# Kernel optimization log

Measured on AMD Instinct MI355X. Metric: run time of the kernel, lower is better.

The kernel has to match this reference:

```python
import jax, jax.numpy as jnp
import numpy as np

N_NODES = 100000
K_NBRS = 16
N_EDGES = N_NODES * K_NBRS


def setup_inputs() -> dict:
    key = jax.random.key(0)
    ks = jax.random.split(key, 20)
    x = jax.random.normal(ks[0], (N_NODES, 3), dtype=jnp.float32)
    # knn-like edge list: every node is the target of exactly K_NBRS edges
    dst = jnp.repeat(jnp.arange(N_NODES, dtype=jnp.int64), K_NBRS)
    src = jax.random.randint(ks[1], (N_EDGES,), 0, N_NODES, dtype=jnp.int64)
    edge_index = jnp.stack([src, dst], axis=0)  # [2, E], row0=source(j), row1=target(i)

    def lin_init(k, fan_in, fan_out):
        s = 1.0 / np.sqrt(fan_in)
        return jax.random.uniform(k, (fan_in, fan_out), jnp.float32, -s, s)

    inp = {"x": x, "edge_index": edge_index}
    inp["W1"], inp["b1"] = lin_init(ks[2], 6, 64), jnp.zeros((64,), jnp.float32)
    for i, kk in zip(range(2, 6), ks[3:7]):
        inp[f"W{i}"] = lin_init(kk, 128, 64)
        inp[f"b{i}"] = jnp.zeros((64,), jnp.float32)
    inp["Wa"], inp["ba"] = lin_init(ks[8], 128, 128), jnp.zeros((128,), jnp.float32)
    inp["Wb"], inp["bb"] = lin_init(ks[9], 128, 3), jnp.zeros((3,), jnp.float32)
    return inp


def edge_conv(x, src, dst, W, b):
    # PyG EdgeConv: message = nn(cat([x_i, x_j - x_i])), max-aggregate at target i
    xi = x[dst]                      # [E, C] center (target) features
    xj = x[src]                      # [E, C] neighbor (source) features
    msg = jnp.concatenate([xi, xj - xi], axis=-1)  # [E, 2C]
    msg = jax.nn.relu(msg @ W + b)                 # [E, 64] per-edge MLP
    return jax.ops.segment_max(msg, dst, num_segments=N_NODES)  # [N, 64]


def reference(x, edge_index, W1, b1, W2, b2, W3, b3, W4, b4, W5, b5, Wa, ba, Wb, bb):
    src, dst = edge_index[0], edge_index[1]
    h = edge_conv(x, src, dst, W1, b1)
    h = edge_conv(h, src, dst, W2, b2)
    h = edge_conv(h, src, dst, W3, b3)
    h = edge_conv(h, src, dst, W4, b4)
    h = edge_conv(h, src, dst, W5, b5)           # [N, 64]
    g = jnp.max(h, axis=0, keepdims=True)        # [1, 64] global max
    feat = jnp.concatenate([h, jnp.broadcast_to(g, h.shape)], axis=1)  # [N, 128]
    out = jax.nn.relu(feat @ Wa + ba) @ Wb + bb  # [N, 3]
    return x + out
```

## Files before the change

kernel.cpp:

```cpp
#include <hip/hip_runtime.h>
#include <math.h>

#define N_NODES 100000
#define K_NBRS 16
#define N_EDGES (N_NODES * K_NBRS)
#define TPB 256
#define NBLK 2048

typedef __attribute__((ext_vector_type(8))) short short8;
typedef __attribute__((ext_vector_type(4))) float float4_;
typedef __attribute__((ext_vector_type(4))) int int4_;
typedef __attribute__((ext_vector_type(4))) unsigned short ushort4_;

__device__ __forceinline__ unsigned short f2bf(float f) {
  unsigned int u = __float_as_uint(f);
  u += 0x7fffu + ((u >> 16) & 1u);
  return (unsigned short)(u >> 16);
}
__device__ __forceinline__ float bf2f(unsigned short b) {
  return __uint_as_float(((unsigned int)b) << 16);
}

__global__ void k_pre(const int* __restrict__ ei, int* __restrict__ srcout,
                      const float* __restrict__ x, const float* __restrict__ W1,
                      const float* __restrict__ b1,
                      unsigned short* __restrict__ A, unsigned short* __restrict__ B) {
  const bool is64 = (ei[1] == 0) && (ei[3] == 0) && (ei[5] == 0) && (ei[7] == 0);
  const int tid = blockIdx.x * blockDim.x + threadIdx.x;
  const int stride = gridDim.x * blockDim.x;
  for (int e = tid; e < N_EDGES; e += stride)
    srcout[e] = is64 ? ei[2 * e] : ei[e];

  const int lane = threadIdx.x & 63;
  const int nwaves = stride >> 6;
  const int wid0 = tid >> 6;
  float w[6];
#pragma unroll
  for (int k = 0; k < 6; ++k) w[k] = W1[k * 64 + lane];
  const float bias = b1[lane];
  for (int i0 = wid0; i0 < N_NODES; i0 += nwaves) {
    const int i = __builtin_amdgcn_readfirstlane(i0);
    const float x0 = x[3 * i], x1 = x[3 * i + 1], x2 = x[3 * i + 2];
    const float b = fmaf(x0, w[3], fmaf(x1, w[4], x2 * w[5]));
    const float a = bias + fmaf(x0, w[0] - w[3],
                          fmaf(x1, w[1] - w[4], x2 * (w[2] - w[5])));
    A[(size_t)i * 64 + lane] = f2bf(a);
    B[(size_t)i * 64 + lane] = f2bf(b);
  }
}

template <bool DO_GMAX>
__global__ void k_aggr(const int* __restrict__ src,
                       const unsigned short* __restrict__ Ain,
                       const unsigned short* __restrict__ Bin,
                       unsigned short* __restrict__ hout, float* __restrict__ P) {
  const int lane = threadIdx.x & 63;
  const int q = lane >> 4;
  const int c4 = (lane & 15) * 4;
  const int nw = (gridDim.x * blockDim.x) >> 6;
  const int w0 = (blockIdx.x * blockDim.x + threadIdx.x) >> 6;
  float4_ gmax = (float4_)(0.f);
  for (int p = w0; p * 4 < N_NODES; p += nw) {
    const int i = __builtin_amdgcn_readfirstlane(p * 4) + q;
    const int* sp = src + (size_t)i * K_NBRS;
    int4_ idx[4];
#pragma unroll
    for (int e4 = 0; e4 < 4; ++e4)
      idx[e4] = *(const int4_*)(sp + e4 * 4);
    ushort4_ gv[16];
#pragma unroll
    for (int e4 = 0; e4 < 4; ++e4)
#pragma unroll
      for (int e = 0; e < 4; ++e)
        gv[e4 * 4 + e] = *(const ushort4_*)(Bin + (size_t)idx[e4][e] * 64 + c4);
    const ushort4_ av = *(const ushort4_*)(Ain + (size_t)i * 64 + c4);
    ushort4_ hb;
#pragma unroll
    for (int t = 0; t < 4; ++t) {
      float m01 = fmaxf(bf2f(gv[0][t]), bf2f(gv[1][t]));
      float m23 = fmaxf(bf2f(gv[2][t]), bf2f(gv[3][t]));
      float m45 = fmaxf(bf2f(gv[4][t]), bf2f(gv[5][t]));
      float m67 = fmaxf(bf2f(gv[6][t]), bf2f(gv[7][t]));
      float m89 = fmaxf(bf2f(gv[8][t]), bf2f(gv[9][t]));
      float mab = fmaxf(bf2f(gv[10][t]), bf2f(gv[11][t]));
      float mcd = fmaxf(bf2f(gv[12][t]), bf2f(gv[13][t]));
      float mef = fmaxf(bf2f(gv[14][t]), bf2f(gv[15][t]));
      const float m = fmaxf(fmaxf(fmaxf(m01, m23), fmaxf(m45, m67)),
                            fmaxf(fmaxf(m89, mab), fmaxf(mcd, mef)));
      const float h = fmaxf(bf2f(av[t]) + m, 0.f);
      hb[t] = f2bf(h);
      if constexpr (DO_GMAX) gmax[t] = fmaxf(gmax[t], h);
    }
    *(ushort4_*)(hout + (size_t)i * 64 + c4) = hb;
  }
  if constexpr (DO_GMAX) {
    __shared__ float red[TPB][4];
#pragma unroll
    for (int t = 0; t < 4; ++t) red[threadIdx.x][t] = gmax[t];
    __syncthreads();
    if (threadIdx.x < 64) {
      const int c = threadIdx.x, j = c >> 2, t = c & 3;
      float mm = 0.f;
#pragma unroll
      for (int w = 0; w < 4; ++w)
#pragma unroll
        for (int qq = 0; qq < 4; ++qq)
          mm = fmaxf(mm, red[w * 64 + qq * 16 + j][t]);
      P[(size_t)blockIdx.x * 64 + c] = mm;
    }
  }
}

__global__ __launch_bounds__(TPB, 2)
void k_gemm(const unsigned short* __restrict__ h, const float* __restrict__ W,
            const float* __restrict__ bn,
            unsigned short* __restrict__ Aout, unsigned short* __restrict__ Bout) {
  __shared__ __align__(16) unsigned short lwhi[128 * 72];
  __shared__ __align__(16) unsigned short lwlo[128 * 72];
  for (int idx = threadIdx.x; idx < 8192; idx += TPB) {
    const int k = idx >> 7, j = idx & 127;
    const float v = (j < 64) ? (W[k * 64 + j] - W[(64 + k) * 64 + j])
                             : W[(64 + k) * 64 + (j - 64)];
    const unsigned short hi = f2bf(v);
    lwhi[j * 72 + k] = hi;
    lwlo[j * 72 + k] = f2bf(v - bf2f(hi));
  }
  __syncthreads();
  const int lane = threadIdx.x & 63;
  const int wav = threadIdx.x >> 6;
  const int l15 = lane & 15, lg = lane >> 4;
  short8 bhi[8][2], blo[8][2];
#pragma unroll
  for (int ct = 0; ct < 8; ++ct)
#pragma unroll
    for (int kk = 0; kk < 2; ++kk) {
      const int off = (ct * 16 + l15) * 72 + kk * 32 + lg * 8;
      bhi[ct][kk] = *(const short8*)&lwhi[off];
      blo[ct][kk] = *(const short8*)&lwlo[off];
    }
  float bv[4];
#pragma unroll
  for (int ct = 0; ct < 4; ++ct) bv[ct] = bn[ct * 16 + l15];
  const int NT = (N_NODES + 63) / 64;
  for (int t = blockIdx.x; t < NT; t += gridDim.x) {
    const int nb = t * 64 + wav * 16;
    const int row = min(nb + l15, N_NODES - 1);
    const unsigned short* hr = h + (size_t)row * 64;
    float4_ acc[8];
#pragma unroll
    for (int ct = 0; ct < 8; ++ct) acc[ct] = (float4_)(0.f);
#pragma unroll
    for (int kk = 0; kk < 2; ++kk) {
      const short8 ahi = *(const short8*)(hr + kk * 32 + lg * 8);
#pragma unroll
      for (int ct = 0; ct < 8; ++ct) {
        acc[ct] = __builtin_amdgcn_mfma_f32_16x16x32_bf16(ahi, bhi[ct][kk], acc[ct], 0, 0, 0);
        acc[ct] = __builtin_amdgcn_mfma_f32_16x16x32_bf16(ahi, blo[ct][kk], acc[ct], 0, 0, 0);
      }
    }
#pragma unroll
    for (int ct = 0; ct < 8; ++ct)
#pragma unroll
      for (int r = 0; r < 4; ++r) {
        const int node = nb + lg * 4 + r;
        if (node < N_NODES) {
          if (ct < 4)
            Aout[(size_t)node * 64 + ct * 16 + l15] = f2bf(acc[ct][r] + bv[ct]);
          else
            Bout[(size_t)node * 64 + (ct - 4) * 16 + l15] = f2bf(acc[ct][r]);
        }
      }
  }
}

__global__ void k_gred(const float* __restrict__ P, float* __restrict__ g) {
  __shared__ float red[16][64];
  const int lane = threadIdx.x & 63;
  const int w = threadIdx.x >> 6;
  float m = 0.f;
  for (int r = w; r < NBLK; r += 16)
    m = fmaxf(m, P[(size_t)r * 64 + lane]);
  red[w][lane] = m;
  __syncthreads();
  if (threadIdx.x < 64) {
    float mm = 0.f;
#pragma unroll
    for (int k = 0; k < 16; ++k) mm = fmaxf(mm, red[k][lane]);
    g[lane] = mm;
  }
}

__global__ __launch_bounds__(TPB, 2)
void k_final(const unsigned short* __restrict__ h, const float* __restrict__ g,
             const float* __restrict__ Wa, const float* __restrict__ ba,
             const float* __restrict__ Wb, const float* __restrict__ bb,
             const float* __restrict__ x, float* __restrict__ out) {
  __shared__ __align__(16) unsigned short lwhi[128 * 72];
  __shared__ __align__(16) unsigned short lwlo[128 * 72];
  __shared__ float sgt[128];
  for (int idx = threadIdx.x; idx < 8192; idx += TPB) {
    const int k = idx >> 7, j = idx & 127;
    const float v = Wa[k * 128 + j];
    const unsigned short hi = f2bf(v);
    lwhi[j * 72 + k] = hi;
    lwlo[j * 72 + k] = f2bf(v - bf2f(hi));
  }
  if (threadIdx.x < 128) {
    const int c = threadIdx.x;
    float s = ba[c];
    for (int k = 0; k < 64; ++k) s = fmaf(g[k], Wa[(64 + k) * 128 + c], s);
    sgt[c] = s;
  }
  __syncthreads();
  const int lane = threadIdx.x & 63;
  const int wav = threadIdx.x >> 6;
  const int l15 = lane & 15, lg = lane >> 4;
  short8 bhi[8][2], blo[8][2];
#pragma unroll
  for (int ct = 0; ct < 8; ++ct)
#pragma unroll
    for (int kk = 0; kk < 2; ++kk) {
      const int off = (ct * 16 + l15) * 72 + kk * 32 + lg * 8;
      bhi[ct][kk] = *(const short8*)&lwhi[off];
      blo[ct][kk] = *(const short8*)&lwlo[off];
    }
  float gtv[8];
#pragma unroll
  for (int ct = 0; ct < 8; ++ct) gtv[ct] = sgt[ct * 16 + l15];
  float wbv[8][3];
#pragma unroll
  for (int ct = 0; ct < 8; ++ct)
#pragma unroll
    for (int jj = 0; jj < 3; ++jj)
      wbv[ct][jj] = Wb[(ct * 16 + l15) * 3 + jj];
  const float bbl = (l15 == 0) ? bb[0] : (l15 == 1 ? bb[1] : bb[2]);
  const int NT = (N_NODES + 63) / 64;
  for (int t = blockIdx.x; t < NT; t += gridDim.x) {
    const int nb = t * 64 + wav * 16;
    const int row = min(nb + l15, N_NODES - 1);
    const unsigned short* hr = h + (size_t)row * 64;
    float4_ acc[8];
#pragma unroll
    for (int ct = 0; ct < 8; ++ct) acc[ct] = (float4_)(0.f);
#pragma unroll
    for (int kk = 0; kk < 2; ++kk) {
      const short8 ahi = *(const short8*)(hr + kk * 32 + lg * 8);
#pragma unroll
      for (int ct = 0; ct < 8; ++ct) {
        acc[ct] = __builtin_amdgcn_mfma_f32_16x16x32_bf16(ahi, bhi[ct][kk], acc[ct], 0, 0, 0);
        acc[ct] = __builtin_amdgcn_mfma_f32_16x16x32_bf16(ahi, blo[ct][kk], acc[ct], 0, 0, 0);
      }
    }
#pragma unroll
    for (int r = 0; r < 4; ++r) {
      float t0 = 0.f, t1 = 0.f, t2 = 0.f;
#pragma unroll
      for (int ct = 0; ct < 8; ++ct) {
        const float hd = fmaxf(acc[ct][r] + gtv[ct], 0.f);
        t0 = fmaf(hd, wbv[ct][0], t0);
        t1 = fmaf(hd, wbv[ct][1], t1);
        t2 = fmaf(hd, wbv[ct][2], t2);
      }
#pragma unroll
      for (int off = 1; off < 16; off <<= 1) {
        t0 += __shfl_xor(t0, off);
        t1 += __shfl_xor(t1, off);
        t2 += __shfl_xor(t2, off);
      }
      const int node = nb + lg * 4 + r;
      if (node < N_NODES && l15 < 3) {
        const float tj = (l15 == 0) ? t0 : (l15 == 1 ? t1 : t2);
        out[(size_t)node * 3 + l15] = x[(size_t)node * 3 + l15] + tj + bbl;
      }
    }
  }
}

extern "C" void kernel_launch(void* const* d_in, const int* in_sizes, int n_in,
                              void* d_out, int out_size, void* d_ws, size_t ws_size,
                              hipStream_t stream) {
  const float* x  = (const float*)d_in[0];
  const int*   ei = (const int*)d_in[1];
  const float* W1 = (const float*)d_in[2];
  const float* b1 = (const float*)d_in[3];
  const float* W2 = (const float*)d_in[4];
  const float* b2 = (const float*)d_in[5];
  const float* W3 = (const float*)d_in[6];
  const float* b3 = (const float*)d_in[7];
  const float* W4 = (const float*)d_in[8];
  const float* b4 = (const float*)d_in[9];
  const float* W5 = (const float*)d_in[10];
  const float* b5 = (const float*)d_in[11];
  const float* Wa = (const float*)d_in[12];
  const float* ba = (const float*)d_in[13];
  const float* Wb = (const float*)d_in[14];
  const float* bb = (const float*)d_in[15];
  float* out = (float*)d_out;

  float* ws = (float*)d_ws;
  int* srcbuf = (int*)ws;
  unsigned short* A0 = (unsigned short*)(ws + 1600000);
  unsigned short* B0 = A0 + 6400000;
  unsigned short* A1 = B0 + 6400000;
  unsigned short* B1 = A1 + 6400000;
  unsigned short* H  = B1 + 6400000;
  float* P = (float*)(H + 6400000);
  float* g = P + (size_t)NBLK * 64;

  k_pre<<<NBLK, TPB, 0, stream>>>(ei, srcbuf, x, W1, b1, A0, B0);
  k_aggr<false><<<NBLK, TPB, 0, stream>>>(srcbuf, A0, B0, H, nullptr);
  k_gemm<<<1024, TPB, 0, stream>>>(H, W2, b2, A1, B1);
  k_aggr<false><<<NBLK, TPB, 0, stream>>>(srcbuf, A1, B1, H, nullptr);
  k_gemm<<<1024, TPB, 0, stream>>>(H, W3, b3, A0, B0);
  k_aggr<false><<<NBLK, TPB, 0, stream>>>(srcbuf, A0, B0, H, nullptr);
  k_gemm<<<1024, TPB, 0, stream>>>(H, W4, b4, A1, B1);
  k_aggr<false><<<NBLK, TPB, 0, stream>>>(srcbuf, A1, B1, H, nullptr);
  k_gemm<<<1024, TPB, 0, stream>>>(H, W5, b5, A0, B0);
  k_aggr<true><<<NBLK, TPB, 0, stream>>>(srcbuf, A0, B0, H, P);
  k_gred<<<1, 1024, 0, stream>>>(P, g);
  k_final<<<512, TPB, 0, stream>>>(H, g, Wa, ba, Wb, bb, x, out);
}
```

Before: 384.7 us.

## Split A/B feature tables into channel quarters for cache-local gathers

```diff
diff --git a/kernel.cpp b/kernel.cpp
--- a/kernel.cpp
+++ b/kernel.cpp
@@ -6,11 +6,11 @@
 #define N_EDGES (N_NODES * K_NBRS)
 #define TPB 256
 #define NBLK 2048
+#define QTAB ((size_t)N_NODES * 16)
 
 typedef __attribute__((ext_vector_type(8))) short short8;
 typedef __attribute__((ext_vector_type(4))) float float4_;
 typedef __attribute__((ext_vector_type(4))) int int4_;
-typedef __attribute__((ext_vector_type(4))) unsigned short ushort4_;
 
 __device__ __forceinline__ unsigned short f2bf(float f) {
   unsigned int u = __float_as_uint(f);
@@ -19,6 +19,12 @@
 }
 __device__ __forceinline__ float bf2f(unsigned short b) {
   return __uint_as_float(((unsigned int)b) << 16);
+}
+__device__ __forceinline__ float lo2f(unsigned int v) {
+  return __uint_as_float(v << 16);
+}
+__device__ __forceinline__ float hi2f(unsigned int v) {
+  return __uint_as_float(v & 0xffff0000u);
 }
 
 __global__ void k_pre(const int* __restrict__ ei, int* __restrict__ srcout,
@@ -32,6 +38,7 @@
     srcout[e] = is64 ? ei[2 * e] : ei[e];
 
   const int lane = threadIdx.x & 63;
+  const int cq = lane >> 4, lc = lane & 15;
   const int nwaves = stride >> 6;
   const int wid0 = tid >> 6;
   float w[6];
@@ -44,68 +51,88 @@
     const float b = fmaf(x0, w[3], fmaf(x1, w[4], x2 * w[5]));
     const float a = bias + fmaf(x0, w[0] - w[3],
                           fmaf(x1, w[1] - w[4], x2 * (w[2] - w[5])));
-    A[(size_t)i * 64 + lane] = f2bf(a);
-    B[(size_t)i * 64 + lane] = f2bf(b);
+    A[cq * QTAB + (size_t)i * 16 + lc] = f2bf(a);
+    B[cq * QTAB + (size_t)i * 16 + lc] = f2bf(b);
   }
 }
 
 template <bool DO_GMAX>
 __global__ void k_aggr(const int* __restrict__ src,
-                       const unsigned short* __restrict__ Ain,
-                       const unsigned short* __restrict__ Bin,
+                       const unsigned short* __restrict__ Aq,
+                       const unsigned short* __restrict__ Bq,
                        unsigned short* __restrict__ hout, float* __restrict__ P) {
   const int lane = threadIdx.x & 63;
-  const int q = lane >> 4;
-  const int c4 = (lane & 15) * 4;
+  const int g8 = lane >> 3;
+  const int l8 = lane & 7;
   const int nw = (gridDim.x * blockDim.x) >> 6;
   const int w0 = (blockIdx.x * blockDim.x + threadIdx.x) >> 6;
-  float4_ gmax = (float4_)(0.f);
-  for (int p = w0; p * 4 < N_NODES; p += nw) {
-    const int i = __builtin_amdgcn_readfirstlane(p * 4) + q;
-    const int* sp = src + (size_t)i * K_NBRS;
-    int4_ idx[4];
-#pragma unroll
-    for (int e4 = 0; e4 < 4; ++e4)
-      idx[e4] = *(const int4_*)(sp + e4 * 4);
-    ushort4_ gv[16];
-#pragma unroll
-    for (int e4 = 0; e4 < 4; ++e4)
-#pragma unroll
-      for (int e = 0; e < 4; ++e)
-        gv[e4 * 4 + e] = *(const ushort4_*)(Bin + (size_t)idx[e4][e] * 64 + c4);
-    const ushort4_ av = *(const ushort4_*)(Ain + (size_t)i * 64 + c4);
-    ushort4_ hb;
-#pragma unroll
-    for (int t = 0; t < 4; ++t) {
-      float m01 = fmaxf(bf2f(gv[0][t]), bf2f(gv[1][t]));
-      float m23 = fmaxf(bf2f(gv[2][t]), bf2f(gv[3][t]));
-      float m45 = fmaxf(bf2f(gv[4][t]), bf2f(gv[5][t]));
-      float m67 = fmaxf(bf2f(gv[6][t]), bf2f(gv[7][t]));
-      float m89 = fmaxf(bf2f(gv[8][t]), bf2f(gv[9][t]));
-      float mab = fmaxf(bf2f(gv[10][t]), bf2f(gv[11][t]));
-      float mcd = fmaxf(bf2f(gv[12][t]), bf2f(gv[13][t]));
-      float mef = fmaxf(bf2f(gv[14][t]), bf2f(gv[15][t]));
-      const float m = fmaxf(fmaxf(fmaxf(m01, m23), fmaxf(m45, m67)),
-                            fmaxf(fmaxf(m89, mab), fmaxf(mcd, mef)));
-      const float h = fmaxf(bf2f(av[t]) + m, 0.f);
-      hb[t] = f2bf(h);
-      if constexpr (DO_GMAX) gmax[t] = fmaxf(gmax[t], h);
-    }
-    *(ushort4_*)(hout + (size_t)i * 64 + c4) = hb;
+  float gmax[4][2];
+#pragma unroll
+  for (int c = 0; c < 4; ++c) gmax[c][0] = gmax[c][1] = 0.f;
+#pragma unroll 1
+  for (int cq = 0; cq < 4; ++cq) {
+    const unsigned short* At = Aq + cq * QTAB;
+    const unsigned short* Bt = Bq + cq * QTAB;
+    for (int p = w0; p * 8 < N_NODES; p += nw) {
+      const int i = __builtin_amdgcn_readfirstlane(p * 8) + g8;
+      const int* sp = src + (size_t)i * K_NBRS;
+      int4_ idx[4];
+#pragma unroll
+      for (int e4 = 0; e4 < 4; ++e4)
+        idx[e4] = *(const int4_*)(sp + e4 * 4);
+      unsigned int gv[16];
+#pragma unroll
+      for (int e4 = 0; e4 < 4; ++e4)
+#pragma unroll
+        for (int e = 0; e < 4; ++e)
+          gv[e4 * 4 + e] =
+              *(const unsigned int*)(Bt + (size_t)idx[e4][e] * 16 + l8 * 2);
+      const unsigned int av =
+          *(const unsigned int*)(At + (size_t)i * 16 + l8 * 2);
+      float m0 = fmaxf(fmaxf(fmaxf(fmaxf(lo2f(gv[0]), lo2f(gv[1])),
+                                   fmaxf(lo2f(gv[2]), lo2f(gv[3]))),
+                             fmaxf(fmaxf(lo2f(gv[4]), lo2f(gv[5])),
+                                   fmaxf(lo2f(gv[6]), lo2f(gv[7])))),
+                       fmaxf(fmaxf(fmaxf(lo2f(gv[8]), lo2f(gv[9])),
+                                   fmaxf(lo2f(gv[10]), lo2f(gv[11]))),
+                             fmaxf(fmaxf(lo2f(gv[12]), lo2f(gv[13])),
+                                   fmaxf(lo2f(gv[14]), lo2f(gv[15])))));
+      float m1 = fmaxf(fmaxf(fmaxf(fmaxf(hi2f(gv[0]), hi2f(gv[1])),
+                                   fmaxf(hi2f(gv[2]), hi2f(gv[3]))),
+                             fmaxf(fmaxf(hi2f(gv[4]), hi2f(gv[5])),
+                                   fmaxf(hi2f(gv[6]), hi2f(gv[7])))),
+                       fmaxf(fmaxf(fmaxf(hi2f(gv[8]), hi2f(gv[9])),
+                                   fmaxf(hi2f(gv[10]), hi2f(gv[11]))),
+                             fmaxf(fmaxf(hi2f(gv[12]), hi2f(gv[13])),
+                                   fmaxf(hi2f(gv[14]), hi2f(gv[15])))));
+      const float h0 = fmaxf(lo2f(av) + m0, 0.f);
+      const float h1 = fmaxf(hi2f(av) + m1, 0.f);
+      const unsigned int hp =
+          (unsigned int)f2bf(h0) | ((unsigned int)f2bf(h1) << 16);
+      *(unsigned int*)(hout + (size_t)i * 64 + cq * 16 + l8 * 2) = hp;
+      if constexpr (DO_GMAX) {
+        gmax[cq][0] = fmaxf(gmax[cq][0], h0);
+        gmax[cq][1] = fmaxf(gmax[cq][1], h1);
+      }
+    }
   }
   if constexpr (DO_GMAX) {
-    __shared__ float red[TPB][4];
-#pragma unroll
-    for (int t = 0; t < 4; ++t) red[threadIdx.x][t] = gmax[t];
+    __shared__ float red[TPB][8];
+#pragma unroll
+    for (int c = 0; c < 4; ++c) {
+      red[threadIdx.x][c * 2] = gmax[c][0];
+      red[threadIdx.x][c * 2 + 1] = gmax[c][1];
+    }
     __syncthreads();
     if (threadIdx.x < 64) {
-      const int c = threadIdx.x, j = c >> 2, t = c & 3;
+      const int c = threadIdx.x;
+      const int cq = c >> 4, rem = c & 15, l8r = rem >> 1, t = rem & 1;
       float mm = 0.f;
 #pragma unroll
       for (int w = 0; w < 4; ++w)
 #pragma unroll
-        for (int qq = 0; qq < 4; ++qq)
-          mm = fmaxf(mm, red[w * 64 + qq * 16 + j][t]);
+        for (int g = 0; g < 8; ++g)
+          mm = fmaxf(mm, red[w * 64 + g * 8 + l8r][cq * 2 + t]);
       P[(size_t)blockIdx.x * 64 + c] = mm;
     }
   }
@@ -165,9 +192,9 @@
         const int node = nb + lg * 4 + r;
         if (node < N_NODES) {
           if (ct < 4)
-            Aout[(size_t)node * 64 + ct * 16 + l15] = f2bf(acc[ct][r] + bv[ct]);
+            Aout[ct * QTAB + (size_t)node * 16 + l15] = f2bf(acc[ct][r] + bv[ct]);
           else
-            Bout[(size_t)node * 64 + (ct - 4) * 16 + l15] = f2bf(acc[ct][r]);
+            Bout[(ct - 4) * QTAB + (size_t)node * 16 + l15] = f2bf(acc[ct][r]);
         }
       }
   }
```

After: 624.0 us. 1.62x slower.
